# Kernel optimization log

Hardware: AMD Instinct MI355X
Metric: run time of the kernel (lower is better)

The kernel has to match this reference:

```python
import jax, jax.numpy as jnp
import numpy as np

K_STEPS = 12
NUM_NEG = 10
B, C, T = 2, 512, 4096


def setup_inputs() -> dict:
    key = jax.random.key(0)
    k0, k1, k2, k3, k4 = jax.random.split(key, 5)
    feat_enc = jax.random.normal(k0, (B, C, T), dtype=jnp.float32)
    feat_context = jax.random.normal(k1, (B, C, T), dtype=jnp.float32)
    W = jax.random.normal(k2, (C, C), dtype=jnp.float32) / np.float32(np.sqrt(C))
    b = jax.random.normal(k3, (C,), dtype=jnp.float32) * 0.01
    # stands in for torch.multinomial draws inside the k-loop: one [T, num_neg]
    # index set per step (values in [0, T))
    neg_idx = jax.random.randint(k4, (K_STEPS, T, NUM_NEG), 0, T, dtype=jnp.int32)
    return {"feat_enc": feat_enc, "feat_context": feat_context, "W": W, "b": b,
            "neg_idx": neg_idx}


def reference(feat_enc, feat_context, W, b, neg_idx):
    # linear over channel dim: (transpose -> Linear -> transpose) == einsum
    c = jnp.einsum('bct,dc->bdt', feat_context, W) + b[None, :, None]  # [B,C,T]
    # cont[b,t,s] = sum_c z[b,c,t] * c[b,c,s]  -> [B,T,T]
    cont = jnp.einsum('bct,bcs->bts', feat_enc, c)
    Bn, Tlen, _ = cont.shape
    total = jnp.zeros((), dtype=cont.dtype)
    for k in range(K_STEPS):
        # positives: diagonal offset=-k -> cont[b, i+k, i], length T-k
        pos = jnp.diagonal(cont, offset=-k, axis1=1, axis2=2)
        pos_loss = jnp.sum(jax.nn.log_sigmoid(pos))
        # torch: neg[b, s, r] = cont[b, s, neg_idx[k, r, s]] for s<num_neg
        idx = neg_idx[k].T  # [num_neg, T]
        idx_b = jnp.broadcast_to(idx[None], (Bn, NUM_NEG, Tlen))
        neg = jnp.take_along_axis(cont[:, :NUM_NEG, :], idx_b, axis=2)
        neg_loss = jnp.sum(jax.nn.log_sigmoid(-neg))
        total = total + pos_loss + NUM_NEG * neg_loss
    return total
```

## Files before the change

kernel.cpp:

```cpp
#include <hip/hip_runtime.h>
#include <hip/hip_bf16.h>

constexpr int KST  = 12;
constexpr int NN   = 10;
constexpr int B    = 2;
constexpr int C    = 512;
constexpr int T    = 4096;
constexpr int BAND = 12;
constexpr int NCH  = C / 32;

typedef float f32x4  __attribute__((ext_vector_type(4)));
typedef short bf16x8 __attribute__((ext_vector_type(8)));
typedef unsigned short u16x8 __attribute__((ext_vector_type(8)));

__device__ __forceinline__ float logsig(float x) {
    return fminf(x, 0.0f) - log1pf(expf(-fabsf(x)));
}
__device__ __forceinline__ unsigned short f2bf(float f) {
    union { float f; unsigned u; } v; v.f = f;
    unsigned r = v.u + 0x7fff + ((v.u >> 16) & 1);
    return (unsigned short)(r >> 16);
}

constexpr int PREP_TRANS_END = 2048;
constexpr int PREP_GRID      = PREP_TRANS_END + (C * C) / (256 * 4);

__global__ __launch_bounds__(256) void prep_all(
    const float* __restrict__ fc, const float* __restrict__ enc,
    const float* __restrict__ W,
    unsigned short* __restrict__ fcp, unsigned short* __restrict__ encp,
    unsigned short* __restrict__ Wp, float* __restrict__ out)
{
    __shared__ float lt[64][65];
    const int bid = blockIdx.x;
    const int tid = threadIdx.x;

    if (bid < PREP_TRANS_END) {
        const int z   = bid >> 9;
        const int rem = bid & 511;
        const int t0  = (rem & 63) * 64;
        const int c0  = (rem >> 6) * 64;
        const float* src = (z < 2 ? fc : enc) + (size_t)(z & 1) * C * T;
        unsigned short* dst =
            (z < 2 ? fcp : encp) + (size_t)(z & 1) * NCH * T * 32;

        const int tq = (tid & 15) * 4;
        const int cr = tid >> 4;
        #pragma unroll
        for (int p = 0; p < 4; ++p) {
            const int c_row = p * 16 + cr;
            const float4 v = *(const float4*)&src[(size_t)(c0 + c_row) * T + t0 + tq];
            lt[tq + 0][c_row] = v.x;
            lt[tq + 1][c_row] = v.y;
            lt[tq + 2][c_row] = v.z;
            lt[tq + 3][c_row] = v.w;
        }
        __syncthreads();

        const int t_row = tid >> 2;
        const int cq    = (tid & 3) * 16;
        u16x8 o0, o1;
        #pragma unroll
        for (int u = 0; u < 8; ++u) o0[u] = f2bf(lt[t_row][cq + u]);
        #pragma unroll
        for (int u = 0; u < 8; ++u) o1[u] = f2bf(lt[t_row][cq + 8 + u]);
        const int cg = c0 + cq;
        const int ks = cg >> 5;
        const int j0 = cg & 31;
        unsigned short* dp = dst + ((size_t)ks * T + t0 + t_row) * 32 + j0;
        *(u16x8*)dp       = o0;
        *(u16x8*)(dp + 8) = o1;
    } else {
        if (bid == PREP_TRANS_END && tid == 0) out[0] = 0.0f;
        const int idx = ((bid - PREP_TRANS_END) * 256 + tid) * 4;
        const int d = idx >> 9;
        const int k = idx & 511;
        const float4 v = *(const float4*)&W[idx];
        ushort4 o;
        o.x = f2bf(v.x); o.y = f2bf(v.y); o.z = f2bf(v.z); o.w = f2bf(v.w);
        *(ushort4*)&Wp[((size_t)(k >> 5) * C + d) * 32 + (k & 31)] = o;
    }
}

__global__ __launch_bounds__(512) void fused_kernel(
    const unsigned short* __restrict__ Wp, const unsigned short* __restrict__ fcp,
    const unsigned short* __restrict__ encp, const float* __restrict__ bias,
    float* __restrict__ negls, float* __restrict__ out)
{
    const int b  = blockIdx.y;
    const int n0 = blockIdx.x * 32;

    __shared__ unsigned short c_t[32 * 512];
    __shared__ float posred[8];

    const int tid  = threadIdx.x;
    const int lane = tid & 63;
    const int w    = tid >> 6;
    const int l15  = lane & 15;
    const int l4   = lane >> 4;
    const int mw   = w * 64;

    const unsigned short* fcpb  = fcp  + (size_t)b * NCH * T * 32;
    const unsigned short* encpb = encp + (size_t)b * NCH * T * 32;

    f32x4 acc[4][2] = {};
    const unsigned short* An  = Wp   + ((size_t)(mw + l15)) * 32 + l4 * 8;
    const unsigned short* Bn0 = fcpb + ((size_t)(n0 + l15)) * 32 + l4 * 8;
    const unsigned short* Bn1 = Bn0 + 16 * 32;

    #pragma unroll 4
    for (int ks = 0; ks < NCH; ++ks) {
        const size_t ao = (size_t)ks * C * 32;
        const size_t bo = (size_t)ks * T * 32;
        const bf16x8 b0 = *(const bf16x8*)(Bn0 + bo);
        const bf16x8 b1 = *(const bf16x8*)(Bn1 + bo);
        #pragma unroll
        for (int i = 0; i < 4; ++i) {
            const bf16x8 a = *(const bf16x8*)(An + ao + (size_t)i * 16 * 32);
            acc[i][0] = __builtin_amdgcn_mfma_f32_16x16x32_bf16(a, b0, acc[i][0], 0, 0, 0);
            acc[i][1] = __builtin_amdgcn_mfma_f32_16x16x32_bf16(a, b1, acc[i][1], 0, 0, 0);
        }
    }

    #pragma unroll
    for (int i = 0; i < 4; ++i) {
        const int mb = mw + i * 16 + l4 * 4;
        const float4 bv = *(const float4*)&bias[mb];
        const int g = mb >> 3;
        #pragma unroll
        for (int j = 0; j < 2; ++j) {
            const int sp = j * 16 + l15;
            ushort4 u;
            u.x = f2bf(acc[i][j][0] + bv.x);
            u.y = f2bf(acc[i][j][1] + bv.y);
            u.z = f2bf(acc[i][j][2] + bv.z);
            u.w = f2bf(acc[i][j][3] + bv.w);
            const int off = sp * 1024 + ((g ^ (sp & 7)) << 4) + ((mb & 4) << 1);
            *(ushort4*)((char*)c_t + off) = u;
        }
    }
    __syncthreads();

    const int i2 = w >> 1;
    const int j2 = w & 1;
    const int rg = i2 * 16 + l15;
    int ti;
    if (rg < 44) { ti = n0 + rg; ti = ti < T ? ti : T - 1; }
    else if (rg < 54) ti = rg - 44;
    else ti = 0;
    const unsigned short* A2p = encpb + (size_t)ti * 32 + l4 * 8;
    const char* B2b = (const char*)c_t + (j2 * 16 + l15) * 1024;
    const int bx2 = l15 & 7;

    f32x4 dacc = {};
    #pragma unroll 4
    for (int ks = 0; ks < NCH; ++ks) {
        const bf16x8 a2 = *(const bf16x8*)(A2p + (size_t)ks * T * 32);
        const int ga = ks * 4 + l4;
        const bf16x8 b2 = *(const bf16x8*)(B2b + ((ga ^ bx2) << 4));
        dacc = __builtin_amdgcn_mfma_f32_16x16x32_bf16(a2, b2, dacc, 0, 0, 0);
    }

    float pos = 0.0f;
    const int colr = j2 * 16 + l15;
    const int scol = n0 + colr;
    #pragma unroll
    for (int r = 0; r < 4; ++r) {
        const int row = i2 * 16 + l4 * 4 + r;
        const float vv = dacc[r];
        if (row < 44) {
            const int k = row - colr;
            if (k >= 0 && k < BAND && scol + k < T) pos += logsig(vv);
        } else if (row < 54) {
            negls[((size_t)b * NN + (row - 44)) * T + scol] = logsig(-vv);
        }
    }
    #pragma unroll
    for (int off = 32; off > 0; off >>= 1) pos += __shfl_down(pos, off, 64);
    if (lane == 0) posred[w] = pos;
    __syncthreads();
    if (tid == 0) {
        float tsum = 0.0f;
        #pragma unroll
        for (int q = 0; q < 8; ++q) tsum += posred[q];
        atomicAdd(out, tsum);
    }
}

__global__ __launch_bounds__(256) void gather_kernel(
    const int4* __restrict__ nidx4, const float* __restrict__ negls,
    float* __restrict__ out)
{
    const int i4 = blockIdx.x * 256 + threadIdx.x;
    const int4 vv = nidx4[i4];
    const int base = i4 * 4;
    const int idxs[4] = {vv.x, vv.y, vv.z, vv.w};
    float local = 0.0f;
    #pragma unroll
    for (int e = 0; e < 4; ++e) {
        const int n = (base + e) % NN;
        local += negls[(size_t)n * T + idxs[e]]
               + negls[(size_t)(NN + n) * T + idxs[e]];
    }
    #pragma unroll
    for (int off = 32; off > 0; off >>= 1) local += __shfl_down(local, off, 64);
    __shared__ float wsum[4];
    if ((threadIdx.x & 63) == 0) wsum[threadIdx.x >> 6] = local;
    __syncthreads();
    if (threadIdx.x == 0)
        atomicAdd(out, (float)NN * (wsum[0] + wsum[1] + wsum[2] + wsum[3]));
}

extern "C" void kernel_launch(void* const* d_in, const int* in_sizes, int n_in,
                              void* d_out, int out_size, void* d_ws, size_t ws_size,
                              hipStream_t stream)
{
    const float* enc  = (const float*)d_in[0];
    const float* fc   = (const float*)d_in[1];
    const float* W    = (const float*)d_in[2];
    const float* bias = (const float*)d_in[3];
    const int4*  nidx4 = (const int4*)d_in[4];
    float* out = (float*)d_out;

    unsigned short* fcp  = (unsigned short*)d_ws;
    unsigned short* encp = fcp  + (size_t)B * NCH * T * 32;
    unsigned short* Wp   = encp + (size_t)B * NCH * T * 32;
    float* negls = (float*)(Wp + (size_t)C * C);

    prep_all<<<PREP_GRID, 256, 0, stream>>>(fc, enc, W, fcp, encp, Wp, out);
    fused_kernel<<<dim3(T / 32, B), 512, 0, stream>>>(Wp, fcp, encp, bias,
                                                      negls, out);
    gather_kernel<<<KST * T * NN / (4 * 256), 256, 0, stream>>>(
        nidx4, negls, out);
}
```

Baseline: 54.84 us.

## Split fused GEMM into standalone c-GEMM plus FP32 CUDA-core band kernel

Stops converting enc to bf16 in the prep kernel and instead reads fp32 enc directly in a new band kernel. That kernel computes the 12 diagonal and 10 negative dot products per column with scalar FMAs and reduces them through LDS. The c = W·fc + b GEMM moves into its own kernel with 64x64 tiles and writes c as bf16 in a [B,C,T] layout to a workspace buffer. This removes the enc transpose/convert pass and the wasted MFMA rows of the band tile. In exchange it adds an extra global round trip for c and a fourth kernel launch.

```diff
diff --git a/kernel.cpp b/kernel.cpp
--- a/kernel.cpp
+++ b/kernel.cpp
@@ -21,28 +21,30 @@
     unsigned r = v.u + 0x7fff + ((v.u >> 16) & 1);
     return (unsigned short)(r >> 16);
 }
-
-constexpr int PREP_TRANS_END = 2048;
+__device__ __forceinline__ float bf2f(unsigned short h) {
+    union { unsigned u; float f; } v; v.u = (unsigned)h << 16;
+    return v.f;
+}
+
+constexpr int PREP_TRANS_END = 1024;
 constexpr int PREP_GRID      = PREP_TRANS_END + (C * C) / (256 * 4);
 
-__global__ __launch_bounds__(256) void prep_all(
-    const float* __restrict__ fc, const float* __restrict__ enc,
-    const float* __restrict__ W,
-    unsigned short* __restrict__ fcp, unsigned short* __restrict__ encp,
-    unsigned short* __restrict__ Wp, float* __restrict__ out)
+__global__ __launch_bounds__(256) void prep(
+    const float* __restrict__ fc, const float* __restrict__ W,
+    unsigned short* __restrict__ fcp, unsigned short* __restrict__ Wp,
+    float* __restrict__ out)
 {
     __shared__ float lt[64][65];
     const int bid = blockIdx.x;
     const int tid = threadIdx.x;
 
     if (bid < PREP_TRANS_END) {
-        const int z   = bid >> 9;
+        const int b   = bid >> 9;
         const int rem = bid & 511;
         const int t0  = (rem & 63) * 64;
         const int c0  = (rem >> 6) * 64;
-        const float* src = (z < 2 ? fc : enc) + (size_t)(z & 1) * C * T;
-        unsigned short* dst =
-            (z < 2 ? fcp : encp) + (size_t)(z & 1) * NCH * T * 32;
+        const float* src = fc + (size_t)b * C * T;
+        unsigned short* dst = fcp + (size_t)b * NCH * T * 32;
 
         const int tq = (tid & 15) * 4;
         const int cr = tid >> 4;
@@ -82,109 +84,129 @@
     }
 }
 
-__global__ __launch_bounds__(512) void fused_kernel(
+__global__ __launch_bounds__(256) void cgemm(
     const unsigned short* __restrict__ Wp, const unsigned short* __restrict__ fcp,
-    const unsigned short* __restrict__ encp, const float* __restrict__ bias,
-    float* __restrict__ negls, float* __restrict__ out)
-{
-    const int b  = blockIdx.y;
-    const int n0 = blockIdx.x * 32;
-
-    __shared__ unsigned short c_t[32 * 512];
-    __shared__ float posred[8];
-
-    const int tid  = threadIdx.x;
-    const int lane = tid & 63;
-    const int w    = tid >> 6;
+    const float* __restrict__ bias, unsigned short* __restrict__ cb)
+{
+    const int b  = blockIdx.z;
+    const int t0 = blockIdx.x * 64;
+    const int d0 = blockIdx.y * 64;
+
+    __shared__ unsigned short c_lds[64][68];
+
+    const int lane = threadIdx.x & 63;
+    const int w    = threadIdx.x >> 6;
+    const int wd   = (w & 1) * 32;
+    const int wt   = (w >> 1) * 32;
     const int l15  = lane & 15;
     const int l4   = lane >> 4;
-    const int mw   = w * 64;
-
-    const unsigned short* fcpb  = fcp  + (size_t)b * NCH * T * 32;
-    const unsigned short* encpb = encp + (size_t)b * NCH * T * 32;
-
-    f32x4 acc[4][2] = {};
-    const unsigned short* An  = Wp   + ((size_t)(mw + l15)) * 32 + l4 * 8;
-    const unsigned short* Bn0 = fcpb + ((size_t)(n0 + l15)) * 32 + l4 * 8;
-    const unsigned short* Bn1 = Bn0 + 16 * 32;
-
+
+    const unsigned short* fcpb = fcp + (size_t)b * NCH * T * 32;
+    const unsigned short* An  = Wp   + (size_t)(d0 + wd + l15) * 32 + l4 * 8;
+    const unsigned short* Bn  = fcpb + (size_t)(t0 + wt + l15) * 32 + l4 * 8;
+
+    f32x4 acc[2][2] = {};
     #pragma unroll 4
     for (int ks = 0; ks < NCH; ++ks) {
         const size_t ao = (size_t)ks * C * 32;
         const size_t bo = (size_t)ks * T * 32;
-        const bf16x8 b0 = *(const bf16x8*)(Bn0 + bo);
-        const bf16x8 b1 = *(const bf16x8*)(Bn1 + bo);
-        #pragma unroll
-        for (int i = 0; i < 4; ++i) {
-            const bf16x8 a = *(const bf16x8*)(An + ao + (size_t)i * 16 * 32);
-            acc[i][0] = __builtin_amdgcn_mfma_f32_16x16x32_bf16(a, b0, acc[i][0], 0, 0, 0);
-            acc[i][1] = __builtin_amdgcn_mfma_f32_16x16x32_bf16(a, b1, acc[i][1], 0, 0, 0);
-        }
-    }
-
-    #pragma unroll
-    for (int i = 0; i < 4; ++i) {
-        const int mb = mw + i * 16 + l4 * 4;
-        const float4 bv = *(const float4*)&bias[mb];
-        const int g = mb >> 3;
+        const bf16x8 a0 = *(const bf16x8*)(An + ao);
+        const bf16x8 a1 = *(const bf16x8*)(An + ao + 16 * 32);
+        const bf16x8 b0 = *(const bf16x8*)(Bn + bo);
+        const bf16x8 b1 = *(const bf16x8*)(Bn + bo + 16 * 32);
+        acc[0][0] = __builtin_amdgcn_mfma_f32_16x16x32_bf16(a0, b0, acc[0][0], 0, 0, 0);
+        acc[0][1] = __builtin_amdgcn_mfma_f32_16x16x32_bf16(a0, b1, acc[0][1], 0, 0, 0);
+        acc[1][0] = __builtin_amdgcn_mfma_f32_16x16x32_bf16(a1, b0, acc[1][0], 0, 0, 0);
+        acc[1][1] = __builtin_amdgcn_mfma_f32_16x16x32_bf16(a1, b1, acc[1][1], 0, 0, 0);
+    }
+
+    #pragma unroll
+    for (int i = 0; i < 2; ++i) {
+        const int drow = wd + i * 16 + l4 * 4;
+        const float4 bv = *(const float4*)&bias[d0 + drow];
+        const float bvr[4] = {bv.x, bv.y, bv.z, bv.w};
         #pragma unroll
         for (int j = 0; j < 2; ++j) {
-            const int sp = j * 16 + l15;
-            ushort4 u;
-            u.x = f2bf(acc[i][j][0] + bv.x);
-            u.y = f2bf(acc[i][j][1] + bv.y);
-            u.z = f2bf(acc[i][j][2] + bv.z);
-            u.w = f2bf(acc[i][j][3] + bv.w);
-            const int off = sp * 1024 + ((g ^ (sp & 7)) << 4) + ((mb & 4) << 1);
-            *(ushort4*)((char*)c_t + off) = u;
-        }
-    }
-    __syncthreads();
-
-    const int i2 = w >> 1;
-    const int j2 = w & 1;
-    const int rg = i2 * 16 + l15;
-    int ti;
-    if (rg < 44) { ti = n0 + rg; ti = ti < T ? ti : T - 1; }
-    else if (rg < 54) ti = rg - 44;
-    else ti = 0;
-    const unsigned short* A2p = encpb + (size_t)ti * 32 + l4 * 8;
-    const char* B2b = (const char*)c_t + (j2 * 16 + l15) * 1024;
-    const int bx2 = l15 & 7;
-
-    f32x4 dacc = {};
+            const int col = wt + j * 16 + l15;
+            #pragma unroll
+            for (int r = 0; r < 4; ++r)
+                c_lds[drow + r][col] = f2bf(acc[i][j][r] + bvr[r]);
+        }
+    }
+    __syncthreads();
+
+    const int row = threadIdx.x >> 2;
+    const int cq  = (threadIdx.x & 3) * 16;
+    const u16x8 o0 = *(const u16x8*)&c_lds[row][cq];
+    const u16x8 o1 = *(const u16x8*)&c_lds[row][cq + 8];
+    unsigned short* dp = cb + (size_t)b * C * T + (size_t)(d0 + row) * T + t0 + cq;
+    *(u16x8*)dp       = o0;
+    *(u16x8*)(dp + 8) = o1;
+}
+
+__global__ __launch_bounds__(256) void band_kernel(
+    const float* __restrict__ enc, const unsigned short* __restrict__ cb,
+    float* __restrict__ negls, float* __restrict__ out)
+{
+    const int b   = blockIdx.y;
+    const int s0  = blockIdx.x * 8;
+    const int tid = threadIdx.x;
+    const int sl  = tid & 7;
+    const int g   = tid >> 3;
+    const int s   = s0 + sl;
+
+    const float* encb = enc + (size_t)b * C * T;
+    const unsigned short* cbb = cb + (size_t)b * C * T;
+
+    float acc[22];
+    #pragma unroll
+    for (int a = 0; a < 22; ++a) acc[a] = 0.0f;
+
     #pragma unroll 4
-    for (int ks = 0; ks < NCH; ++ks) {
-        const bf16x8 a2 = *(const bf16x8*)(A2p + (size_t)ks * T * 32);
-        const int ga = ks * 4 + l4;
-        const bf16x8 b2 = *(const bf16x8*)(B2b + ((ga ^ bx2) << 4));
-        dacc = __builtin_amdgcn_mfma_f32_16x16x32_bf16(a2, b2, dacc, 0, 0, 0);
-    }
+    for (int dd = 0; dd < 16; ++dd) {
+        const int d = g * 16 + dd;
+        const float* er = encb + (size_t)d * T;
+        const float cc = bf2f(cbb[(size_t)d * T + s]);
+        #pragma unroll
+        for (int k = 0; k < BAND; ++k) {
+            int t = s + k; t = t < T ? t : T - 1;
+            acc[k] += er[t] * cc;
+        }
+        const float4 e0 = *(const float4*)&er[0];
+        const float4 e1 = *(const float4*)&er[4];
+        const float2 e2 = *(const float2*)&er[8];
+        acc[12] += e0.x * cc; acc[13] += e0.y * cc;
+        acc[14] += e0.z * cc; acc[15] += e0.w * cc;
+        acc[16] += e1.x * cc; acc[17] += e1.y * cc;
+        acc[18] += e1.z * cc; acc[19] += e1.w * cc;
+        acc[20] += e2.x * cc; acc[21] += e2.y * cc;
+    }
+
+    __shared__ float red[32][22][9];
+    #pragma unroll
+    for (int a = 0; a < 22; ++a) red[g][a][sl] = acc[a];
+    __syncthreads();
 
     float pos = 0.0f;
-    const int colr = j2 * 16 + l15;
-    const int scol = n0 + colr;
-    #pragma unroll
-    for (int r = 0; r < 4; ++r) {
-        const int row = i2 * 16 + l4 * 4 + r;
-        const float vv = dacc[r];
-        if (row < 44) {
-            const int k = row - colr;
-            if (k >= 0 && k < BAND && scol + k < T) pos += logsig(vv);
-        } else if (row < 54) {
-            negls[((size_t)b * NN + (row - 44)) * T + scol] = logsig(-vv);
+    if (tid < 176) {
+        const int a   = tid >> 3;
+        const int sl2 = tid & 7;
+        const int s2  = s0 + sl2;
+        float v = 0.0f;
+        #pragma unroll
+        for (int gg = 0; gg < 32; ++gg) v += red[gg][a][sl2];
+        if (a < BAND) {
+            if (s2 + a < T) pos = logsig(v);
+        } else {
+            negls[((size_t)b * NN + (a - BAND)) * T + s2] = logsig(-v);
         }
     }
     #pragma unroll
     for (int off = 32; off > 0; off >>= 1) pos += __shfl_down(pos, off, 64);
-    if (lane == 0) posred[w] = pos;
-    __syncthreads();
-    if (tid == 0) {
-        float tsum = 0.0f;
-        #pragma unroll
-        for (int q = 0; q < 8; ++q) tsum += posred[q];
-        atomicAdd(out, tsum);
-    }
+    __shared__ float wsum[4];
+    if ((tid & 63) == 0) wsum[tid >> 6] = pos;
+    __syncthreads();
+    if (tid == 0) atomicAdd(out, wsum[0] + wsum[1] + wsum[2] + wsum[3]);
 }
 
 __global__ __launch_bounds__(256) void gather_kernel(
@@ -222,14 +244,14 @@
     const int4*  nidx4 = (const int4*)d_in[4];
     float* out = (float*)d_out;
 
-    unsigned short* fcp  = (unsigned short*)d_ws;
-    unsigned short* encp = fcp  + (size_t)B * NCH * T * 32;
-    unsigned short* Wp   = encp + (size_t)B * NCH * T * 32;
-    float* negls = (float*)(Wp + (size_t)C * C);
-
-    prep_all<<<PREP_GRID, 256, 0, stream>>>(fc, enc, W, fcp, encp, Wp, out);
-    fused_kernel<<<dim3(T / 32, B), 512, 0, stream>>>(Wp, fcp, encp, bias,
-                                                      negls, out);
+    unsigned short* fcp = (unsigned short*)d_ws;
+    unsigned short* Wp  = fcp + (size_t)B * NCH * T * 32;
+    unsigned short* cbuf = Wp + (size_t)C * C;
+    float* negls = (float*)(cbuf + (size_t)B * C * T);
+
+    prep<<<PREP_GRID, 256, 0, stream>>>(fc, W, fcp, Wp, out);
+    cgemm<<<dim3(T / 64, C / 64, B), 256, 0, stream>>>(Wp, fcp, bias, cbuf);
+    band_kernel<<<dim3(T / 8, B), 256, 0, stream>>>(enc, cbuf, negls, out);
     gather_kernel<<<KST * T * NN / (4 * 256), 256, 0, stream>>>(
         nidx4, negls, out);
 }
```

Measured after the change: 85.89 us. +56.6%, slower.

## Split fused GEMM+band kernel into separate linear GEMM and band kernels

Applied to the files above, without the earlier changes.

Replaces the fused kernel, where each 32-column block computed the full 512-row projection into LDS, with a standalone tiled GEMM that writes the projected context to a global bf16 packed buffer. A second band kernel then reads that buffer directly for the diagonal-band and negative dot products. This spreads the projection over many more 64x64 tiles instead of 256 large blocks, aiming for better occupancy and load balance. The cost is an extra kernel launch and a global round-trip of the projected tensor.

```diff
diff --git a/kernel.cpp b/kernel.cpp
--- a/kernel.cpp
+++ b/kernel.cpp
@@ -82,15 +82,76 @@
     }
 }
 
-__global__ __launch_bounds__(512) void fused_kernel(
+__global__ __launch_bounds__(256) void cgemm(
     const unsigned short* __restrict__ Wp, const unsigned short* __restrict__ fcp,
-    const unsigned short* __restrict__ encp, const float* __restrict__ bias,
+    const float* __restrict__ bias, unsigned short* __restrict__ cpk)
+{
+    const int b  = blockIdx.z;
+    const int t0 = blockIdx.x * 64;
+    const int d0 = blockIdx.y * 64;
+
+    __shared__ unsigned short c_lds[64][68];
+
+    const int lane = threadIdx.x & 63;
+    const int w    = threadIdx.x >> 6;
+    const int wt   = (w >> 1) * 32;
+    const int wd   = (w & 1) * 32;
+    const int l15  = lane & 15;
+    const int l4   = lane >> 4;
+
+    const unsigned short* fcpb = fcp + (size_t)b * NCH * T * 32;
+    const unsigned short* An = fcpb + (size_t)(t0 + wt + l15) * 32 + l4 * 8;
+    const unsigned short* Bn = Wp   + (size_t)(d0 + wd + l15) * 32 + l4 * 8;
+
+    f32x4 acc[2][2] = {};
+    #pragma unroll 4
+    for (int ks = 0; ks < NCH; ++ks) {
+        const size_t ao = (size_t)ks * T * 32;
+        const size_t bo = (size_t)ks * C * 32;
+        const bf16x8 a0 = *(const bf16x8*)(An + ao);
+        const bf16x8 a1 = *(const bf16x8*)(An + ao + 16 * 32);
+        const bf16x8 b0 = *(const bf16x8*)(Bn + bo);
+        const bf16x8 b1 = *(const bf16x8*)(Bn + bo + 16 * 32);
+        acc[0][0] = __builtin_amdgcn_mfma_f32_16x16x32_bf16(a0, b0, acc[0][0], 0, 0, 0);
+        acc[0][1] = __builtin_amdgcn_mfma_f32_16x16x32_bf16(a0, b1, acc[0][1], 0, 0, 0);
+        acc[1][0] = __builtin_amdgcn_mfma_f32_16x16x32_bf16(a1, b0, acc[1][0], 0, 0, 0);
+        acc[1][1] = __builtin_amdgcn_mfma_f32_16x16x32_bf16(a1, b1, acc[1][1], 0, 0, 0);
+    }
+
+    #pragma unroll
+    for (int j = 0; j < 2; ++j) {
+        const int dcol = wd + j * 16 + l15;
+        const float bv = bias[d0 + dcol];
+        #pragma unroll
+        for (int i = 0; i < 2; ++i) {
+            const int trow = wt + i * 16 + l4 * 4;
+            #pragma unroll
+            for (int r = 0; r < 4; ++r)
+                c_lds[trow + r][dcol] = f2bf(acc[i][j][r] + bv);
+        }
+    }
+    __syncthreads();
+
+    {
+        const int t     = threadIdx.x >> 2;
+        const int piece = threadIdx.x & 3;
+        const int ks    = (d0 >> 5) + (piece >> 1);
+        const int inner = (piece & 1) * 16;
+        const u16x8 o0 = *(const u16x8*)&c_lds[t][piece * 16];
+        const u16x8 o1 = *(const u16x8*)&c_lds[t][piece * 16 + 8];
+        unsigned short* dp = cpk + (size_t)b * NCH * T * 32
+                           + ((size_t)ks * T + t0 + t) * 32 + inner;
+        *(u16x8*)dp       = o0;
+        *(u16x8*)(dp + 8) = o1;
+    }
+}
+
+__global__ __launch_bounds__(512) void band_kernel(
+    const unsigned short* __restrict__ encp, const unsigned short* __restrict__ cpk,
     float* __restrict__ negls, float* __restrict__ out)
 {
     const int b  = blockIdx.y;
     const int n0 = blockIdx.x * 32;
-
-    __shared__ unsigned short c_t[32 * 512];
     __shared__ float posred[8];
 
     const int tid  = threadIdx.x;
@@ -98,48 +159,9 @@
     const int w    = tid >> 6;
     const int l15  = lane & 15;
     const int l4   = lane >> 4;
-    const int mw   = w * 64;
-
-    const unsigned short* fcpb  = fcp  + (size_t)b * NCH * T * 32;
+
     const unsigned short* encpb = encp + (size_t)b * NCH * T * 32;
-
-    f32x4 acc[4][2] = {};
-    const unsigned short* An  = Wp   + ((size_t)(mw + l15)) * 32 + l4 * 8;
-    const unsigned short* Bn0 = fcpb + ((size_t)(n0 + l15)) * 32 + l4 * 8;
-    const unsigned short* Bn1 = Bn0 + 16 * 32;
-
-    #pragma unroll 4
-    for (int ks = 0; ks < NCH; ++ks) {
-        const size_t ao = (size_t)ks * C * 32;
-        const size_t bo = (size_t)ks * T * 32;
-        const bf16x8 b0 = *(const bf16x8*)(Bn0 + bo);
-        const bf16x8 b1 = *(const bf16x8*)(Bn1 + bo);
-        #pragma unroll
-        for (int i = 0; i < 4; ++i) {
-            const bf16x8 a = *(const bf16x8*)(An + ao + (size_t)i * 16 * 32);
-            acc[i][0] = __builtin_amdgcn_mfma_f32_16x16x32_bf16(a, b0, acc[i][0], 0, 0, 0);
-            acc[i][1] = __builtin_amdgcn_mfma_f32_16x16x32_bf16(a, b1, acc[i][1], 0, 0, 0);
-        }
-    }
-
-    #pragma unroll
-    for (int i = 0; i < 4; ++i) {
-        const int mb = mw + i * 16 + l4 * 4;
-        const float4 bv = *(const float4*)&bias[mb];
-        const int g = mb >> 3;
-        #pragma unroll
-        for (int j = 0; j < 2; ++j) {
-            const int sp = j * 16 + l15;
-            ushort4 u;
-            u.x = f2bf(acc[i][j][0] + bv.x);
-            u.y = f2bf(acc[i][j][1] + bv.y);
-            u.z = f2bf(acc[i][j][2] + bv.z);
-            u.w = f2bf(acc[i][j][3] + bv.w);
-            const int off = sp * 1024 + ((g ^ (sp & 7)) << 4) + ((mb & 4) << 1);
-            *(ushort4*)((char*)c_t + off) = u;
-        }
-    }
-    __syncthreads();
+    const unsigned short* cpkb  = cpk  + (size_t)b * NCH * T * 32;
 
     const int i2 = w >> 1;
     const int j2 = w & 1;
@@ -149,15 +171,14 @@
     else if (rg < 54) ti = rg - 44;
     else ti = 0;
     const unsigned short* A2p = encpb + (size_t)ti * 32 + l4 * 8;
-    const char* B2b = (const char*)c_t + (j2 * 16 + l15) * 1024;
-    const int bx2 = l15 & 7;
+    const unsigned short* B2p = cpkb + (size_t)(n0 + j2 * 16 + l15) * 32 + l4 * 8;
 
     f32x4 dacc = {};
     #pragma unroll 4
     for (int ks = 0; ks < NCH; ++ks) {
-        const bf16x8 a2 = *(const bf16x8*)(A2p + (size_t)ks * T * 32);
-        const int ga = ks * 4 + l4;
-        const bf16x8 b2 = *(const bf16x8*)(B2b + ((ga ^ bx2) << 4));
+        const size_t o = (size_t)ks * T * 32;
+        const bf16x8 a2 = *(const bf16x8*)(A2p + o);
+        const bf16x8 b2 = *(const bf16x8*)(B2p + o);
         dacc = __builtin_amdgcn_mfma_f32_16x16x32_bf16(a2, b2, dacc, 0, 0, 0);
     }
 
@@ -225,11 +246,12 @@
     unsigned short* fcp  = (unsigned short*)d_ws;
     unsigned short* encp = fcp  + (size_t)B * NCH * T * 32;
     unsigned short* Wp   = encp + (size_t)B * NCH * T * 32;
-    float* negls = (float*)(Wp + (size_t)C * C);
+    unsigned short* cpk  = Wp   + (size_t)C * C;
+    float* negls = (float*)(cpk + (size_t)B * NCH * T * 32);
 
     prep_all<<<PREP_GRID, 256, 0, stream>>>(fc, enc, W, fcp, encp, Wp, out);
-    fused_kernel<<<dim3(T / 32, B), 512, 0, stream>>>(Wp, fcp, encp, bias,
-                                                      negls, out);
+    cgemm<<<dim3(T / 64, C / 64, B), 256, 0, stream>>>(Wp, fcp, bias, cpk);
+    band_kernel<<<dim3(T / 32, B), 512, 0, stream>>>(encp, cpk, negls, out);
     gather_kernel<<<KST * T * NN / (4 * 256), 256, 0, stream>>>(
         nidx4, negls, out);
 }
```

After: 54.77 us. About the same (-0.1%).

## Replace negative gather with index histogram weighting fused into main kernel

Applied to the files above, without the earlier changes.

Adds blocks to the prep kernel that build, per negative row, a histogram of how often each column index is sampled across all steps. The fused GEMM kernel then multiplies each negative log-sigmoid by its count and adds it to the block's sum, so the separate gather kernel and its intermediate buffer go away. This removes one launch and the scattered global reads, at the cost of shared-memory atomics in ten long-running prep blocks.

```diff
diff --git a/kernel.cpp b/kernel.cpp
--- a/kernel.cpp
+++ b/kernel.cpp
@@ -23,15 +23,20 @@
 }
 
 constexpr int PREP_TRANS_END = 2048;
-constexpr int PREP_GRID      = PREP_TRANS_END + (C * C) / (256 * 4);
+constexpr int PREP_CAST_END  = PREP_TRANS_END + (C * C) / (256 * 4);
+constexpr int PREP_GRID      = PREP_CAST_END + NN;
 
 __global__ __launch_bounds__(256) void prep_all(
     const float* __restrict__ fc, const float* __restrict__ enc,
-    const float* __restrict__ W,
+    const float* __restrict__ W, const int* __restrict__ nidx,
     unsigned short* __restrict__ fcp, unsigned short* __restrict__ encp,
-    unsigned short* __restrict__ Wp, float* __restrict__ out)
+    unsigned short* __restrict__ Wp, int* __restrict__ cnt,
+    float* __restrict__ out)
 {
-    __shared__ float lt[64][65];
+    __shared__ char smem[64 * 65 * 4];
+    float (*lt)[65] = (float (*)[65])smem;
+    int* hist = (int*)smem;
+
     const int bid = blockIdx.x;
     const int tid = threadIdx.x;
 
@@ -70,7 +75,7 @@
         unsigned short* dp = dst + ((size_t)ks * T + t0 + t_row) * 32 + j0;
         *(u16x8*)dp       = o0;
         *(u16x8*)(dp + 8) = o1;
-    } else {
+    } else if (bid < PREP_CAST_END) {
         if (bid == PREP_TRANS_END && tid == 0) out[0] = 0.0f;
         const int idx = ((bid - PREP_TRANS_END) * 256 + tid) * 4;
         const int d = idx >> 9;
@@ -79,13 +84,23 @@
         ushort4 o;
         o.x = f2bf(v.x); o.y = f2bf(v.y); o.z = f2bf(v.z); o.w = f2bf(v.w);
         *(ushort4*)&Wp[((size_t)(k >> 5) * C + d) * 32 + (k & 31)] = o;
+    } else {
+        const int n = bid - PREP_CAST_END;
+        for (int s = tid; s < T; s += 256) hist[s] = 0;
+        __syncthreads();
+        for (int j = tid; j < KST * T; j += 256) {
+            const int v = nidx[j * NN + n];
+            atomicAdd(&hist[v], 1);
+        }
+        __syncthreads();
+        for (int s = tid; s < T; s += 256) cnt[n * T + s] = hist[s];
     }
 }
 
 __global__ __launch_bounds__(512) void fused_kernel(
     const unsigned short* __restrict__ Wp, const unsigned short* __restrict__ fcp,
     const unsigned short* __restrict__ encp, const float* __restrict__ bias,
-    float* __restrict__ negls, float* __restrict__ out)
+    const int* __restrict__ cnt, float* __restrict__ out)
 {
     const int b  = blockIdx.y;
     const int n0 = blockIdx.x * 32;
@@ -172,7 +187,8 @@
             const int k = row - colr;
             if (k >= 0 && k < BAND && scol + k < T) pos += logsig(vv);
         } else if (row < 54) {
-            negls[((size_t)b * NN + (row - 44)) * T + scol] = logsig(-vv);
+            const int c = cnt[(row - 44) * T + scol];
+            pos += (float)(NN * c) * logsig(-vv);
         }
     }
     #pragma unroll
@@ -185,30 +201,6 @@
         for (int q = 0; q < 8; ++q) tsum += posred[q];
         atomicAdd(out, tsum);
     }
-}
-
-__global__ __launch_bounds__(256) void gather_kernel(
-    const int4* __restrict__ nidx4, const float* __restrict__ negls,
-    float* __restrict__ out)
-{
-    const int i4 = blockIdx.x * 256 + threadIdx.x;
-    const int4 vv = nidx4[i4];
-    const int base = i4 * 4;
-    const int idxs[4] = {vv.x, vv.y, vv.z, vv.w};
-    float local = 0.0f;
-    #pragma unroll
-    for (int e = 0; e < 4; ++e) {
-        const int n = (base + e) % NN;
-        local += negls[(size_t)n * T + idxs[e]]
-               + negls[(size_t)(NN + n) * T + idxs[e]];
-    }
-    #pragma unroll
-    for (int off = 32; off > 0; off >>= 1) local += __shfl_down(local, off, 64);
-    __shared__ float wsum[4];
-    if ((threadIdx.x & 63) == 0) wsum[threadIdx.x >> 6] = local;
-    __syncthreads();
-    if (threadIdx.x == 0)
-        atomicAdd(out, (float)NN * (wsum[0] + wsum[1] + wsum[2] + wsum[3]));
 }
 
 extern "C" void kernel_launch(void* const* d_in, const int* in_sizes, int n_in,
@@ -219,17 +211,16 @@
     const float* fc   = (const float*)d_in[1];
     const float* W    = (const float*)d_in[2];
     const float* bias = (const float*)d_in[3];
-    const int4*  nidx4 = (const int4*)d_in[4];
+    const int*   nidx = (const int*)d_in[4];
     float* out = (float*)d_out;
 
     unsigned short* fcp  = (unsigned short*)d_ws;
     unsigned short* encp = fcp  + (size_t)B * NCH * T * 32;
     unsigned short* Wp   = encp + (size_t)B * NCH * T * 32;
-    float* negls = (float*)(Wp + (size_t)C * C);
-
-    prep_all<<<PREP_GRID, 256, 0, stream>>>(fc, enc, W, fcp, encp, Wp, out);
+    int* cnt = (int*)(Wp + (size_t)C * C);
+
+    prep_all<<<PREP_GRID, 256, 0, stream>>>(fc, enc, W, nidx,
+                                            fcp, encp, Wp, cnt, out);
     fused_kernel<<<dim3(T / 32, B), 512, 0, stream>>>(Wp, fcp, encp, bias,
-                                                      negls, out);
-    gather_kernel<<<KST * T * NN / (4 * 256), 256, 0, stream>>>(
-        nidx4, negls, out);
-}
+                                                      cnt, out);
+}
```

Measured after the change: 95.98 us. 1.75x slower.
